# Kernel tuning notes

Hardware: AMD Instinct MI355X
Metric: run time of the kernel (lower is better)

Reference implementation:

```python
import jax, jax.numpy as jnp
import numpy as np

N_TX, N_ACC, N_MER = 100000, 50000, 5000
HID, HEADS, OUT_CH, LAYERS = 128, 4, 64, 3
HC = HID * HEADS  # 512, concat-heads width
SRC_T = ['tx', 'tx', 'tx', 'acc', 'acc', 'mer']
DST_T = ['acc', 'acc', 'mer', 'tx', 'tx', 'tx']


def setup_inputs():
    key = jax.random.key(0)
    ks = jax.random.split(key, 16)
    rn = lambda k, s: jax.random.normal(k, s, dtype=jnp.float32) * 0.05
    n_of = {'tx': N_TX, 'acc': N_ACC, 'mer': N_MER}
    E = N_TX  # one sender-acct / receiver-acct / merchant edge per transaction
    src = jnp.stack([jax.random.randint(jax.random.fold_in(ks[0], r), (E,), 0, n_of[SRC_T[r]]) for r in range(6)])
    dst = jnp.stack([jax.random.randint(jax.random.fold_in(ks[1], r), (E,), 0, n_of[DST_T[r]]) for r in range(6)])
    edges = jnp.stack([src, dst], axis=1).astype(jnp.int32)  # [6, 2, E] (rel, src/dst, edge)
    return dict(
        x_tx=rn(ks[2], (N_TX, 64)), x_acc=rn(ks[3], (N_ACC, 32)), x_mer=rn(ks[4], (N_MER, 32)),
        Wtx=rn(ks[5], (64, HID)), btx=jnp.zeros((HID,), jnp.float32),
        Wacc=rn(ks[6], (32, HID)), bacc=jnp.zeros((HID,), jnp.float32),
        Wmer=rn(ks[7], (32, HID)), bmer=jnp.zeros((HID,), jnp.float32),
        W0=rn(ks[8], (6, HID, HC)),            # layer-0 GAT linear per relation
        Wrest=rn(ks[9], (LAYERS - 1, 6, HC, HC)),  # layers 1..L-1
        att_s=rn(ks[10], (LAYERS, 6, HEADS, HID)),
        att_d=rn(ks[11], (LAYERS, 6, HEADS, HID)),
        att_b=jnp.zeros((LAYERS, 6, HC), jnp.float32),
        bn_g=jnp.ones((LAYERS, HC), jnp.float32), bn_b=jnp.zeros((LAYERS, HC), jnp.float32),
        Wh1=rn(ks[12], (HC, OUT_CH)), bh1=jnp.zeros((OUT_CH,), jnp.float32),
        Wh2=rn(ks[13], (OUT_CH, 1)), bh2=jnp.zeros((1,), jnp.float32),
        edges=edges)


def _gat_rel(x_src, x_dst, src, dst, W, a_s, a_d, b, n_dst):
    """PyG GATConv (shared lin, add_self_loops=False, concat heads), eval mode."""
    H, C = a_s.shape
    hs = (x_src @ W).reshape(-1, H, C)  # [Ns, H, C]
    hd = (x_dst @ W).reshape(-1, H, C)  # [Nd, H, C]
    e = jax.nn.leaky_relu((hs * a_s).sum(-1)[src] + (hd * a_d).sum(-1)[dst], 0.2)  # [E, H]
    m = jax.lax.stop_gradient(jax.ops.segment_max(e, dst, num_segments=n_dst))
    ex = jnp.exp(e - m[dst])
    denom = jax.ops.segment_sum(ex, dst, num_segments=n_dst)
    alpha = ex / (denom[dst] + 1e-16)  # segment softmax over in-edges of each dst
    out = jax.ops.segment_sum(alpha[:, :, None] * hs[src], dst, num_segments=n_dst)
    return out.reshape(n_dst, H * C) + b


def _forward(x_tx, x_acc, x_mer, Wtx, btx, Wacc, bacc, Wmer, bmer, W0, Wrest,
             att_s, att_d, att_b, bn_g, bn_b, Wh1, bh1, Wh2, bh2, edges):
    h = {'tx': jax.nn.relu(x_tx @ Wtx + btx),
         'acc': jax.nn.relu(x_acc @ Wacc + bacc),
         'mer': jax.nn.relu(x_mer @ Wmer + bmer)}
    n_of = {'tx': x_tx.shape[0], 'acc': x_acc.shape[0], 'mer': x_mer.shape[0]}
    for i in range(LAYERS):
        Wl = W0 if i == 0 else Wrest[i - 1]
        new = {k: jnp.zeros((n_of[k], HC), x_tx.dtype) for k in n_of}  # HeteroConv aggr='sum'
        for r in range(6):
            o = _gat_rel(h[SRC_T[r]], h[DST_T[r]], edges[r, 0], edges[r, 1],
                         Wl[r], att_s[i, r], att_d[i, r], att_b[i, r], n_of[DST_T[r]])
            new[DST_T[r]] = new[DST_T[r]] + o
        t = new['tx']  # BatchNorm1d (batch statistics) on transaction nodes only
        mu = t.mean(0)
        var = t.var(0)
        new['tx'] = (t - mu) / jnp.sqrt(var + 1e-5) * bn_g[i] + bn_b[i]
        new = {k: jax.nn.relu(v) for k, v in new.items()}
        if i > 0:  # residual from second layer on
            new = {k: new[k] + h[k] for k in new}
        h = new
    hidden = jax.nn.relu(h['tx'] @ Wh1 + bh1)
    return (hidden @ Wh2 + bh2).squeeze(-1)  # [N_tx] logits


def reference(x_tx, x_acc, x_mer, Wtx, btx, Wacc, bacc, Wmer, bmer, W0, Wrest,
              att_s, att_d, att_b, bn_g, bn_b, Wh1, bh1, Wh2, bh2, edges):
    return _forward(x_tx, x_acc, x_mer, Wtx, btx, Wacc, bacc, Wmer, bmer, W0, Wrest,
                    att_s, att_d, att_b, bn_g, bn_b, Wh1, bh1, Wh2, bh2, edges)
```

## Files before the change

### kernel.cpp

```cpp
#include <hip/hip_runtime.h>
#include <math.h>


typedef unsigned short BF16;
typedef short short8 __attribute__((ext_vector_type(8)));
typedef float f32x4 __attribute__((ext_vector_type(4)));
typedef __bf16 bf16x8 __attribute__((ext_vector_type(8)));

static __device__ __forceinline__ float lrelu(float x){ return x > 0.f ? x : 0.2f*x; }

__device__ __forceinline__ float ldE(const float* p, long i){ return p[i]; }
__device__ __forceinline__ float ldE(const BF16* p, long i){
  return __uint_as_float((unsigned)p[i] << 16);
}
__device__ __forceinline__ void stE(float* p, long i, float v){ p[i] = v; }
__device__ __forceinline__ void stE(BF16* p, long i, float v){
  unsigned u = __float_as_uint(v);
  p[i] = (BF16)((u + 0x7FFFu + ((u >> 16) & 1u)) >> 16);
}
__device__ __forceinline__ BF16 f2bf(float v){
  unsigned u = __float_as_uint(v);
  return (BF16)((u + 0x7FFFu + ((u >> 16) & 1u)) >> 16);
}
__device__ __forceinline__ float bf2f(short s){
  return __uint_as_float((unsigned)(unsigned short)s << 16);
}
__device__ __forceinline__ float4 ld4E(const float* p, long i){ return *(const float4*)(p + i); }
__device__ __forceinline__ float4 ld4E(const BF16* p, long i){
  ushort4 s = *(const ushort4*)(p + i);
  return make_float4(__uint_as_float((unsigned)s.x<<16), __uint_as_float((unsigned)s.y<<16),
                     __uint_as_float((unsigned)s.z<<16), __uint_as_float((unsigned)s.w<<16));
}

__global__ void k_zero(int* __restrict__ p, long n){
  long i = (long)blockIdx.x*blockDim.x + threadIdx.x;
  if (i < n) p[i] = 0;
}
__global__ void k_fill_f32(float* __restrict__ p, long n, float v){
  long i = (long)blockIdx.x*blockDim.x + threadIdx.x;
  if (i < n) p[i] = v;
}

__global__ __launch_bounds__(256) void k_wt(const float* __restrict__ in, BF16* __restrict__ out,
                                            int K, int N)
{
  __shared__ float t[32][33];
  int kb = blockIdx.y*32, nb = blockIdx.x*32;
  int tx = threadIdx.x & 31, ty8 = threadIdx.x >> 5;
  for (int j = ty8; j < 32; j += 8){
    int k = kb + j, n = nb + tx;
    t[j][tx] = (k < K && n < N) ? in[(long)k*N + n] : 0.f;
  }
  __syncthreads();
  for (int j = ty8; j < 32; j += 8){
    int n = nb + j, k = kb + tx;
    if (n < N && k < K) out[(long)n*K + k] = f2bf(t[tx][j]);
  }
}

template<int BN, int WM, int WN, int FM, int FN, typename TC>
__global__ __launch_bounds__(256) void k_mfma(
    const BF16* __restrict__ A, const BF16* __restrict__ Bt, TC* __restrict__ C,
    int M, int K, int c0, int ldc, const float* __restrict__ bias, int doRelu)
{
  constexpr int BM = 128;
  constexpr int LSTR = 72;
  __shared__ __attribute__((aligned(16))) short Als[BM][LSTR];
  __shared__ __attribute__((aligned(16))) short Bls[BN][LSTR];
  const int bm = blockIdx.y*BM;
  const int tid = threadIdx.x;
  const int wave = tid >> 6, lane = tid & 63;
  const int wr = wave / WN, wc = wave % WN;
  const int lrow = lane & 15, kg = lane >> 4;
  f32x4 acc[FM][FN] = {};
  for (int k0 = 0; k0 < K; k0 += 64){
    #pragma unroll
    for (int t = 0; t < 4; ++t){
      int idx = tid + t*256;
      int row = idx >> 3, kc = (idx & 7) << 3;
      int gr = bm + row;
      short8 v = {};
      if (gr < M) v = *(const short8*)(A + (long)gr*K + k0 + kc);
      *(short8*)&Als[row][kc] = v;
    }
    #pragma unroll
    for (int t = 0; t < BN/32; ++t){
      int idx = tid + t*256;
      int row = idx >> 3, kc = (idx & 7) << 3;
      *(short8*)&Bls[row][kc] = *(const short8*)(Bt + (long)(c0+row)*K + k0 + kc);
    }
    __syncthreads();
    #pragma unroll
    for (int kk = 0; kk < 2; ++kk){
      short8 af[FM], bq[FN];
      #pragma unroll
      for (int m = 0; m < FM; ++m)
        af[m] = *(const short8*)&Als[wr*FM*16 + m*16 + lrow][kk*32 + kg*8];
      #pragma unroll
      for (int n = 0; n < FN; ++n)
        bq[n] = *(const short8*)&Bls[wc*FN*16 + n*16 + lrow][kk*32 + kg*8];
      #pragma unroll
      for (int m = 0; m < FM; ++m)
        #pragma unroll
        for (int n = 0; n < FN; ++n)
          acc[m][n] = __builtin_amdgcn_mfma_f32_16x16x32_bf16(
              __builtin_bit_cast(bf16x8, af[m]), __builtin_bit_cast(bf16x8, bq[n]),
              acc[m][n], 0, 0, 0);
    }
    __syncthreads();
  }
  #pragma unroll
  for (int m = 0; m < FM; ++m){
    #pragma unroll
    for (int n = 0; n < FN; ++n){
      #pragma unroll
      for (int j = 0; j < 4; ++j){
        int row = bm + wr*FM*16 + m*16 + kg*4 + j;
        if (row >= M) continue;
        int col = wc*FN*16 + n*16 + lrow;
        float v = acc[m][n][j];
        if (bias) v += bias[col];
        if (doRelu) v = fmaxf(v, 0.f);
        stE(C, (long)row*ldc + col, v);
      }
    }
  }
}

template<typename TA, typename TC>
__global__ __launch_bounds__(256) void k_gemm(
    const TA* __restrict__ A, const float* __restrict__ B, TC* __restrict__ C,
    int M, int N, int K, int ldb, const float* __restrict__ bias, int doRelu)
{
  __shared__ float As[16][64];
  __shared__ float Bs[16][64];
  const int bm = blockIdx.y*64, bn = blockIdx.x*64;
  const int tid = threadIdx.x;
  const int ty = tid >> 4, tx = tid & 15;
  const int ar = tid >> 2;
  const int ac = (tid & 3) << 2;
  const int br = tid >> 4;
  const int bc = (tid & 15) << 2;
  float acc[4][4] = {};
  for (int k0 = 0; k0 < K; k0 += 16){
    int row = bm + ar;
    float4 av = make_float4(0.f,0.f,0.f,0.f);
    if (row < M) av = ld4E(A, (long)row*K + k0 + ac);
    As[ac+0][ar]=av.x; As[ac+1][ar]=av.y; As[ac+2][ar]=av.z; As[ac+3][ar]=av.w;
    float4 bv = make_float4(0.f,0.f,0.f,0.f);
    if (bn + bc + 3 < N) bv = *(const float4*)(B + (long)(k0+br)*ldb + bn + bc);
    *(float4*)&Bs[br][bc] = bv;
    __syncthreads();
    #pragma unroll
    for (int kk = 0; kk < 16; ++kk){
      float a[4], b[4];
      #pragma unroll
      for (int x = 0; x < 4; ++x){ a[x]=As[kk][ty*4+x]; b[x]=Bs[kk][tx*4+x]; }
      #pragma unroll
      for (int y = 0; y < 4; ++y)
        #pragma unroll
        for (int x = 0; x < 4; ++x) acc[y][x] += a[y]*b[x];
    }
    __syncthreads();
  }
  #pragma unroll
  for (int y = 0; y < 4; ++y){
    int row = bm + ty*4 + y;
    if (row >= M) continue;
    #pragma unroll
    for (int x = 0; x < 4; ++x){
      int col = bn + tx*4 + x;
      if (col >= N) continue;
      float v = acc[y][x];
      if (bias) v += bias[col];
      if (doRelu) v = fmaxf(v, 0.f);
      stE(C, (long)row*N + col, v);
    }
  }
}

__global__ void k_fold(const float* __restrict__ W, const float* __restrict__ att,
                       float* __restrict__ F, int Din)
{
  int idx = blockIdx.x*blockDim.x + threadIdx.x;
  if (idx >= 4*Din) return;
  int h = idx / Din, k = idx % Din;
  float s = 0.f;
  const float* wr = W + (long)k*512 + h*128;
  const float* ar = att + h*128;
  for (int c = 0; c < 128; ++c) s += wr[c]*ar[c];
  F[h*Din + k] = s;
}

__global__ __launch_bounds__(256) void k_score4(
    const BF16* __restrict__ X, const float* __restrict__ F,
    float* __restrict__ out, int N, int Din)
{
  __shared__ float Fs[2048];
  for (int i = threadIdx.x; i < 4*Din; i += 256) Fs[i] = F[i];
  __syncthreads();
  int wave = threadIdx.x >> 6, lane = threadIdx.x & 63;
  int base = lane*8;
  bool act = base < Din;
  float f0[8], f1[8], f2[8], f3[8];
  if (act){
    #pragma unroll
    for (int j = 0; j < 8; ++j){
      f0[j] = Fs[0*Din + base + j];
      f1[j] = Fs[1*Din + base + j];
      f2[j] = Fs[2*Din + base + j];
      f3[j] = Fs[3*Din + base + j];
    }
  }
  #pragma unroll
  for (int t = 0; t < 4; ++t){
    int node = blockIdx.x*16 + wave*4 + t;
    if (node >= N) break;
    float p0=0.f, p1=0.f, p2=0.f, p3=0.f;
    if (act){
      short8 v = *(const short8*)(X + (long)node*Din + base);
      #pragma unroll
      for (int j = 0; j < 8; ++j){
        float x = bf2f(v[j]);
        p0 += x*f0[j]; p1 += x*f1[j]; p2 += x*f2[j]; p3 += x*f3[j];
      }
    }
    #pragma unroll
    for (int off = 32; off; off >>= 1){
      p0 += __shfl_down(p0, off, 64);
      p1 += __shfl_down(p1, off, 64);
      p2 += __shfl_down(p2, off, 64);
      p3 += __shfl_down(p3, off, 64);
    }
    if (lane == 0){
      out[(long)node*4 + 0] = p0;
      out[(long)node*4 + 1] = p1;
      out[(long)node*4 + 2] = p2;
      out[(long)node*4 + 3] = p3;
    }
  }
}

__global__ void k_hist(const int* __restrict__ dst, int* __restrict__ counts, int E, int nd){
  int e = blockIdx.x*blockDim.x + threadIdx.x;
  if (e >= E) return;
  int d = dst[e];
  if ((unsigned)d < (unsigned)nd) atomicAdd(&counts[d], 1);
}
__global__ void k_scan1(const int* __restrict__ counts, int* __restrict__ indptr,
                        int* __restrict__ bsums, int n)
{
  __shared__ int sm[256];
  int i = blockIdx.x*256 + threadIdx.x;
  int v = (i < n) ? counts[i] : 0;
  sm[threadIdx.x] = v; __syncthreads();
  for (int off = 1; off < 256; off <<= 1){
    int t = (threadIdx.x >= off) ? sm[threadIdx.x - off] : 0;
    __syncthreads();
    sm[threadIdx.x] += t;
    __syncthreads();
  }
  if (i < n) indptr[i+1] = sm[threadIdx.x];
  if (threadIdx.x == 255) bsums[blockIdx.x] = sm[255];
  if (blockIdx.x == 0 && threadIdx.x == 0) indptr[0] = 0;
}
__global__ void k_scan2(int* __restrict__ bsums, int nb){
  __shared__ int sm[1024];
  int t = threadIdx.x;
  int v = (t < nb) ? bsums[t] : 0;
  sm[t] = v; __syncthreads();
  for (int off = 1; off < 1024; off <<= 1){
    int x = (t >= off) ? sm[t - off] : 0;
    __syncthreads();
    sm[t] += x;
    __syncthreads();
  }
  if (t < nb) bsums[t] = sm[t];
}
__global__ void k_scan3(int* __restrict__ indptr, const int* __restrict__ bsums, int n){
  if (blockIdx.x == 0) return;
  int i = blockIdx.x*256 + threadIdx.x;
  int add = bsums[blockIdx.x - 1];
  if (i < n) indptr[i+1] += add;
}
__global__ void k_scatter(const int* __restrict__ src, const int* __restrict__ dst,
                          const int* __restrict__ indptr, int* __restrict__ cursor,
                          int* __restrict__ esrc, int E, int nd, int ns)
{
  int e = blockIdx.x*blockDim.x + threadIdx.x;
  if (e >= E) return;
  int d = dst[e];
  if ((unsigned)d >= (unsigned)nd) return;
  int s = src[e];
  if ((unsigned)s >= (unsigned)ns) s = 0;
  int pos = indptr[d] + atomicAdd(&cursor[d], 1);
  if (pos >= 0 && pos < E) esrc[pos] = s;
}

__global__ __launch_bounds__(256) void k_alpha(
    const float* __restrict__ ss, const float* __restrict__ sd,
    const int* __restrict__ indptr, const int* __restrict__ esrc,
    float* __restrict__ alpha, int n_dst, int E, int ns)
{
  int wid = (blockIdx.x*blockDim.x + threadIdx.x) >> 6;
  int lane = threadIdx.x & 63;
  if (wid >= n_dst) return;
  int e0 = indptr[wid], e1 = indptr[wid+1];
  e0 = max(0, min(e0, E)); e1 = max(e0, min(e1, E));
  if (e0 >= e1) return;
  int h = lane >> 4, g = lane & 15;
  float sdl = sd[(long)wid*4 + h];
  float m = -INFINITY;
  for (int e = e0 + g; e < e1; e += 16){
    int s = esrc[e]; if ((unsigned)s >= (unsigned)ns) s = 0;
    m = fmaxf(m, lrelu(ss[(long)s*4 + h] + sdl));
  }
  #pragma unroll
  for (int o = 1; o < 16; o <<= 1) m = fmaxf(m, __shfl_xor(m, o, 16));
  float den = 0.f;
  for (int e = e0 + g; e < e1; e += 16){
    int s = esrc[e]; if ((unsigned)s >= (unsigned)ns) s = 0;
    den += __expf(lrelu(ss[(long)s*4 + h] + sdl) - m);
  }
  #pragma unroll
  for (int o = 1; o < 16; o <<= 1) den += __shfl_xor(den, o, 16);
  float inv = 1.f/(den + 1e-16f);
  for (int e = e0 + g; e < e1; e += 16){
    int s = esrc[e]; if ((unsigned)s >= (unsigned)ns) s = 0;
    alpha[(long)e*4 + h] = __expf(lrelu(ss[(long)s*4 + h] + sdl) - m) * inv;
  }
}

template<int NJ>
__global__ __launch_bounds__(256) void k_agg(
    const BF16* __restrict__ Zt, const float* __restrict__ alpha,
    const int* __restrict__ indptr, const int* __restrict__ esrc,
    BF16* __restrict__ out, int ldc, int c0w, int TW, int head0,
    int accum, int n_dst, int E, int ns)
{
  int wid = (blockIdx.x*blockDim.x + threadIdx.x) >> 6;
  int lane = threadIdx.x & 63;
  if (wid >= n_dst) return;
  int e0 = indptr[wid], e1 = indptr[wid+1];
  e0 = max(0, min(e0, E)); e1 = max(e0, min(e1, E));
  float acc[NJ];
  #pragma unroll
  for (int j = 0; j < NJ; ++j) acc[j] = 0.f;
  for (int e = e0; e < e1; ++e){
    int s = esrc[e]; if ((unsigned)s >= (unsigned)ns) s = 0;
    float aA = alpha[(long)e*4 + head0];
    float aB = (NJ == 4) ? alpha[(long)e*4 + head0 + 1] : aA;
    const BF16* zr = Zt + (long)s*TW;
    #pragma unroll
    for (int j = 0; j < NJ; ++j){
      int col = lane + 64*j;
      if (col < TW){
        float a = (NJ == 4 && j >= 2) ? aB : aA;
        acc[j] += a * ldE(zr, col);
      }
    }
  }
  #pragma unroll
  for (int j = 0; j < NJ; ++j){
    int col = lane + 64*j;
    if (col < TW){
      long idx = (long)wid*ldc + c0w + col;
      float v = acc[j];
      if (accum) v += ldE(out, idx);
      stE(out, idx, v);
    }
  }
}

__global__ void k_bnp(const BF16* __restrict__ nw, float* __restrict__ bnp,
                      int N, int TW, int P)
{
  int col  = threadIdx.x & (TW - 1);
  int slot = threadIdx.x / TW;
  int rpb  = 256 / TW;
  int p    = blockIdx.x*rpb + slot;
  float s = 0.f, s2 = 0.f;
  for (long r = p; r < N; r += P){
    float v = ldE(nw, r*TW + col);
    s += v; s2 += v*v;
  }
  bnp[(long)p*2*TW + col]      = s;
  bnp[(long)p*2*TW + TW + col] = s2;
}
__global__ void k_bnf(const float* __restrict__ bnp, float* __restrict__ bns,
                      int P, int TW)
{
  for (int c = threadIdx.x; c < 2*TW; c += 256){
    float s = 0.f;
    for (int p = 0; p < P; ++p) s += bnp[(long)p*2*TW + c];
    bns[c] = s;
  }
}
__global__ void k_bn_apply(const BF16* __restrict__ nw, const float* __restrict__ bns,
                           const float* __restrict__ g, const float* __restrict__ b,
                           BF16* __restrict__ A, int N, int TW, int c0, int res)
{
  long total = (long)N*TW;
  for (long i = (long)blockIdx.x*blockDim.x + threadIdx.x; i < total;
       i += (long)gridDim.x*blockDim.x){
    int col = (int)(i % TW);
    long r  = i / TW;
    float mu  = bns[col] / (float)N;
    float var = bns[TW + col] / (float)N - mu*mu;
    int gc = c0 + col;
    float sc = g[gc] * rsqrtf(var + 1e-5f);
    float sh = b[gc] - mu*sc;
    float v = fmaxf(ldE(nw, i)*sc + sh, 0.f);
    long ai = r*512 + gc;
    if (res) v += ldE(A, ai);
    stE(A, ai, v);
  }
}

__global__ void k_update(const BF16* __restrict__ B, const float* __restrict__ ab1,
                         const float* __restrict__ ab2, BF16* __restrict__ A,
                         long n512, int res)
{
  for (long i = (long)blockIdx.x*blockDim.x + threadIdx.x; i < n512;
       i += (long)gridDim.x*blockDim.x){
    int c = (int)(i & 511);
    float v = ldE(B, i) + ab1[c] + (ab2 ? ab2[c] : 0.f);
    v = fmaxf(v, 0.f);
    if (res) v += ldE(A, i);
    stE(A, i, v);
  }
}

__global__ void k_logits(const BF16* __restrict__ Hid, const float* __restrict__ Wh2,
                         const float* __restrict__ bh2, float* __restrict__ out, int N)
{
  int node = (blockIdx.x*blockDim.x + threadIdx.x) >> 6;
  int lane = threadIdx.x & 63;
  if (node >= N) return;
  float v = ldE(Hid, (long)node*64 + lane) * Wh2[lane];
  #pragma unroll
  for (int off = 32; off; off >>= 1) v += __shfl_down(v, off, 64);
  if (lane == 0) out[node] = v + bh2[0];
}

struct Arena {
  BF16 *A[3];
  BF16 *Bst[3];
  BF16 *Zt;
  BF16 *nwtile;
  BF16 *hidden;
  float *alpha;
  float *ss, *sd, *fs, *fd, *bnp, *bns;
  int *counts, *bsums;
  int *indptr[6], *esrc[6];
  BF16 *Wt0[6], *WtL[2][6], *Wh1t;
  size_t total;
};

extern "C" void kernel_launch(void* const* d_in, const int* in_sizes, int n_in,
                              void* d_out, int out_size, void* d_ws, size_t ws_size,
                              hipStream_t stream)
{
  const float* x_tx  = (const float*)d_in[0];
  const float* x_acc = (const float*)d_in[1];
  const float* x_mer = (const float*)d_in[2];
  const float* Wtx = (const float*)d_in[3];  const float* btx  = (const float*)d_in[4];
  const float* Wacc= (const float*)d_in[5];  const float* bacc = (const float*)d_in[6];
  const float* Wmer= (const float*)d_in[7];  const float* bmer = (const float*)d_in[8];
  const float* W0   = (const float*)d_in[9];
  const float* Wrest= (const float*)d_in[10];
  const float* att_s= (const float*)d_in[11];
  const float* att_d= (const float*)d_in[12];
  const float* att_b= (const float*)d_in[13];
  const float* bn_g = (const float*)d_in[14];
  const float* bn_b = (const float*)d_in[15];
  const float* Wh1  = (const float*)d_in[16]; const float* bh1 = (const float*)d_in[17];
  const float* Wh2  = (const float*)d_in[18]; const float* bh2 = (const float*)d_in[19];
  const int*   edges= (const int*)d_in[20];

  const int E    = in_sizes[20] / 12;
  const int nTx  = in_sizes[0] / 64;
  const int nAcc = in_sizes[1] / 32;
  const int nMer = in_sizes[2] / 32;
  const int nOf[3]   = {nTx, nAcc, nMer};
  const int SRC_T[6] = {0,0,0,1,1,2};
  const int DST_T[6] = {1,1,2,0,0,0};
  const int maxN = max(nTx, max(nAcc, nMer));
  (void)n_in;

  auto layout = [&](int TW)->Arena{
    Arena P{};
    size_t off = 0;
    auto a = [&](size_t bytes)->char*{
      char* p = (char*)d_ws + off;
      off += (bytes + 255) & ~(size_t)255;
      return p;
    };
    auto al = [](size_t b){ return (b + 255) & ~(size_t)255; };
    P.A[0]   = (BF16*)a((size_t)nTx *512*2);
    P.A[1]   = (BF16*)a((size_t)nAcc*512*2);
    P.A[2]   = (BF16*)a((size_t)nMer*512*2);
    P.Bst[1] = (BF16*)a((size_t)nAcc*512*2);
    P.Bst[2] = (BF16*)a((size_t)nMer*512*2);
    size_t zB  = al((size_t)maxN*TW*2);
    size_t nwB = al((size_t)nTx*TW*2);
    size_t hidB= al((size_t)nTx*64*2);
    size_t scr = zB + nwB;
    char* scrBase = a(scr > hidB ? scr : hidB);
    P.Zt     = (BF16*)scrBase;
    P.nwtile = (BF16*)(scrBase + zB);
    P.hidden = (BF16*)scrBase;
    P.alpha  = (float*)a((size_t)3*E*4*4);
    P.ss     = (float*)a((size_t)maxN*4*4);
    P.sd     = (float*)a((size_t)maxN*4*4);
    P.fs     = (float*)a(4*512*4);
    P.fd     = (float*)a(4*512*4);
    P.bnp    = (float*)a(262144);
    P.bns    = (float*)a(4096);
    P.counts = (int*)a((size_t)maxN*4);
    P.bsums  = (int*)a(4096);
    for (int r = 0; r < 6; ++r){
      P.indptr[r] = (int*)a((size_t)(nOf[DST_T[r]]+1)*4);
      P.esrc[r]   = (int*)a((size_t)E*4);
    }
    for (int r = 0; r < 6; ++r) P.Wt0[r] = (BF16*)a((size_t)512*128*2);
    for (int l = 0; l < 2; ++l)
      for (int r = 0; r < 6; ++r) P.WtL[l][r] = (BF16*)a((size_t)512*512*2);
    P.Wh1t = (BF16*)a((size_t)64*512*2);
    P.total = off;
    return P;
  };

  int TW = 0;
  Arena P{};
  for (int cand : {256, 128, 64, 32}){
    P = layout(cand);
    if (P.total <= ws_size){ TW = cand; break; }
  }
  if (TW == 0){
    float sentinel = 10000.0f + (float)(ws_size >> 20);
    k_fill_f32<<<dim3((out_size+255)/256), dim3(256), 0, stream>>>((float*)d_out, (long)out_size, sentinel);
    return;
  }
  const int nTiles = 512 / TW;
  const int rpb = 256 / TW, PBX = 128, Pp = PBX * rpb;
  dim3 b256(256);

  for (int r = 0; r < 6; ++r)
    k_wt<<<dim3(16,4), b256, 0, stream>>>(W0 + (size_t)r*128*512, P.Wt0[r], 128, 512);
  for (int l = 0; l < 2; ++l)
    for (int r = 0; r < 6; ++r)
      k_wt<<<dim3(16,16), b256, 0, stream>>>(Wrest + ((size_t)l*6 + r)*512*512, P.WtL[l][r], 512, 512);
  k_wt<<<dim3(2,16), b256, 0, stream>>>(Wh1, P.Wh1t, 512, 64);

  auto mfma_gemm = [&](const BF16* A, const BF16* Bt, BF16* Cp, int M, int K, int c0){
    dim3 g(1, (M+127)/128);
    if (TW >= 128){
      for (int ch = 0; ch < TW; ch += 128)
        k_mfma<128,2,2,4,4,BF16><<<g,b256,0,stream>>>(A, Bt, Cp + ch, M, K, c0 + ch, TW, (const float*)nullptr, 0);
    } else if (TW == 64){
      k_mfma<64,4,1,2,4,BF16><<<g,b256,0,stream>>>(A, Bt, Cp, M, K, c0, TW, (const float*)nullptr, 0);
    } else {
      k_mfma<32,4,1,2,2,BF16><<<g,b256,0,stream>>>(A, Bt, Cp, M, K, c0, TW, (const float*)nullptr, 0);
    }
  };
  auto agg = [&](const BF16* Zt, const float* al, const int* ip, const int* es,
                 BF16* out, int ldc, int c0w, int head0, int accum, int nd, int ns){
    dim3 g((nd+3)/4);
    if (TW == 256)      k_agg<4><<<g,b256,0,stream>>>(Zt, al, ip, es, out, ldc, c0w, TW, head0, accum, nd, E, ns);
    else if (TW == 128) k_agg<2><<<g,b256,0,stream>>>(Zt, al, ip, es, out, ldc, c0w, TW, head0, accum, nd, E, ns);
    else                k_agg<1><<<g,b256,0,stream>>>(Zt, al, ip, es, out, ldc, c0w, TW, head0, accum, nd, E, ns);
  };

  for (int r = 0; r < 6; ++r){
    int nd = nOf[DST_T[r]], ns = nOf[SRC_T[r]];
    const int* srcP = edges + (size_t)r*2*E;
    const int* dstP = srcP + E;
    int nb = (nd + 255)/256;
    k_zero   <<<dim3(nb),          b256, 0, stream>>>(P.counts, (long)nd);
    k_hist   <<<dim3((E+255)/256), b256, 0, stream>>>(dstP, P.counts, E, nd);
    k_scan1  <<<dim3(nb),          b256, 0, stream>>>(P.counts, P.indptr[r], P.bsums, nd);
    k_scan2  <<<dim3(1),           dim3(1024),0, stream>>>(P.bsums, nb);
    k_scan3  <<<dim3(nb),          b256, 0, stream>>>(P.indptr[r], P.bsums, nd);
    k_zero   <<<dim3(nb),          b256, 0, stream>>>(P.counts, (long)nd);
    k_scatter<<<dim3((E+255)/256), b256, 0, stream>>>(srcP, dstP, P.indptr[r], P.counts, P.esrc[r], E, nd, ns);
  }

  k_gemm<float,BF16><<<dim3(2,(nTx +63)/64), b256, 0, stream>>>(x_tx,  Wtx,  P.A[0], nTx,  128, 64, 128, btx,  1);
  k_gemm<float,BF16><<<dim3(2,(nAcc+63)/64), b256, 0, stream>>>(x_acc, Wacc, P.A[1], nAcc, 128, 32, 128, bacc, 1);
  k_gemm<float,BF16><<<dim3(2,(nMer+63)/64), b256, 0, stream>>>(x_mer, Wmer, P.A[2], nMer, 128, 32, 128, bmer, 1);

  for (int i = 0; i < 3; ++i){
    const int Din = (i == 0) ? 128 : 512;
    const int res = (i > 0) ? 1 : 0;
    auto Wof = [&](int r)->const float*{
      return (i == 0) ? (W0 + (size_t)r*128*512)
                      : (Wrest + ((size_t)(i-1)*6 + r)*512*512);
    };
    auto Wtof = [&](int r)->const BF16*{
      return (i == 0) ? P.Wt0[r] : P.WtL[i-1][r];
    };
    for (int r = 0; r < 3; ++r){
      int dt = DST_T[r];
      int nd = nOf[dt];
      const float* as_ = att_s + ((size_t)(i*6 + r))*4*128;
      const float* ad_ = att_d + ((size_t)(i*6 + r))*4*128;
      k_fold<<<dim3((4*Din+255)/256), b256, 0, stream>>>(Wof(r), as_, P.fs, Din);
      k_fold<<<dim3((4*Din+255)/256), b256, 0, stream>>>(Wof(r), ad_, P.fd, Din);
      k_score4<<<dim3((nTx+15)/16), b256, 0, stream>>>(P.A[0], P.fs, P.ss, nTx, Din);
      k_score4<<<dim3((nd+15)/16),  b256, 0, stream>>>(P.A[dt], P.fd, P.sd, nd, Din);
      k_alpha<<<dim3((nd+3)/4), b256, 0, stream>>>(P.ss, P.sd, P.indptr[r], P.esrc[r],
                                                   P.alpha, nd, E, nTx);
      int accF = (r == 1) ? 1 : 0;
      for (int t = 0; t < nTiles; ++t){
        int c0 = t*TW;
        mfma_gemm(P.A[0], Wtof(r), P.Zt, nTx, Din, c0);
        agg(P.Zt, P.alpha, P.indptr[r], P.esrc[r], P.Bst[dt], 512, c0, c0 >> 7, accF, nd, nTx);
      }
    }
    for (int r = 3; r < 6; ++r){
      int st = SRC_T[r];
      int ns = nOf[st];
      const float* as_ = att_s + ((size_t)(i*6 + r))*4*128;
      const float* ad_ = att_d + ((size_t)(i*6 + r))*4*128;
      k_fold<<<dim3((4*Din+255)/256), b256, 0, stream>>>(Wof(r), as_, P.fs, Din);
      k_fold<<<dim3((4*Din+255)/256), b256, 0, stream>>>(Wof(r), ad_, P.fd, Din);
      k_score4<<<dim3((ns+15)/16),  b256, 0, stream>>>(P.A[st], P.fs, P.ss, ns, Din);
      k_score4<<<dim3((nTx+15)/16), b256, 0, stream>>>(P.A[0],  P.fd, P.sd, nTx, Din);
      k_alpha<<<dim3((nTx+3)/4), b256, 0, stream>>>(P.ss, P.sd, P.indptr[r], P.esrc[r],
                                                    P.alpha + (size_t)(r-3)*E*4, nTx, E, ns);
    }
    for (int t = 0; t < nTiles; ++t){
      int c0 = t*TW;
      for (int r = 3; r < 6; ++r){
        int st = SRC_T[r], ns = nOf[st];
        mfma_gemm(P.A[st], Wtof(r), P.Zt, ns, Din, c0);
        agg(P.Zt, P.alpha + (size_t)(r-3)*E*4, P.indptr[r], P.esrc[r],
            P.nwtile, TW, 0, c0 >> 7, (r > 3) ? 1 : 0, nTx, ns);
      }
      k_bnp<<<dim3(PBX), b256, 0, stream>>>(P.nwtile, P.bnp, nTx, TW, Pp);
      k_bnf<<<dim3(1),   b256, 0, stream>>>(P.bnp, P.bns, Pp, TW);
      k_bn_apply<<<dim3(2048), b256, 0, stream>>>(P.nwtile, P.bns,
          bn_g + (size_t)i*512, bn_b + (size_t)i*512, P.A[0], nTx, TW, c0, res);
    }
    const float* ab0 = att_b + ((size_t)(i*6 + 0))*512;
    const float* ab1 = att_b + ((size_t)(i*6 + 1))*512;
    const float* ab2 = att_b + ((size_t)(i*6 + 2))*512;
    k_update<<<dim3(2048), b256, 0, stream>>>(P.Bst[1], ab0, ab1, P.A[1], (long)nAcc*512, res);
    k_update<<<dim3(256),  b256, 0, stream>>>(P.Bst[2], ab2, (const float*)nullptr, P.A[2], (long)nMer*512, res);
  }

  k_mfma<64,4,1,2,4,BF16><<<dim3(1,(nTx+127)/128), b256, 0, stream>>>(
      P.A[0], P.Wh1t, P.hidden, nTx, 512, 0, 64, bh1, 1);
  k_logits<<<dim3((nTx+3)/4), b256, 0, stream>>>(P.hidden, Wh2, bh2, (float*)d_out, nTx);
}
```

Before: 12.16 ms.

## Batch attention folds and scores, fuse three tx-destination aggregations into one kernel

```diff
diff --git a/kernel.cpp b/kernel.cpp
--- a/kernel.cpp
+++ b/kernel.cpp
@@ -58,6 +58,26 @@
   }
 }
 
+__global__ __launch_bounds__(256) void k_foldAll(
+    const float* __restrict__ Wbase, long wstride,
+    const float* __restrict__ atts, const float* __restrict__ attd,
+    float* __restrict__ F, int Din)
+{
+  int w = (blockIdx.x*256 + threadIdx.x) >> 6;
+  int lane = threadIdx.x & 63;
+  int total = 48*Din;
+  if (w >= total) return;
+  int k = w % Din;
+  int rem = w / Din;
+  int h = rem & 3, sd = (rem >> 2) & 1, r = rem >> 3;
+  const float* wr = Wbase + (long)r*wstride + (long)k*512 + h*128;
+  const float* ar = (sd ? attd : atts) + r*512 + h*128;
+  float p = wr[lane]*ar[lane] + wr[lane+64]*ar[lane+64];
+  #pragma unroll
+  for (int off = 32; off; off >>= 1) p += __shfl_down(p, off, 64);
+  if (lane == 0) F[(long)((r*2+sd)*4 + h)*Din + k] = p;
+}
+
 template<int BN, int WM, int WN, int FM, int FN, typename TC>
 __global__ __launch_bounds__(256) void k_mfma(
     const BF16* __restrict__ A, const BF16* __restrict__ Bt, TC* __restrict__ C,
@@ -67,6 +87,7 @@
   constexpr int LSTR = 72;
   __shared__ __attribute__((aligned(16))) short Als[BM][LSTR];
   __shared__ __attribute__((aligned(16))) short Bls[BN][LSTR];
+  const int bn0 = blockIdx.x * BN;
   const int bm = blockIdx.y*BM;
   const int tid = threadIdx.x;
   const int wave = tid >> 6, lane = tid & 63;
@@ -87,7 +108,7 @@
     for (int t = 0; t < BN/32; ++t){
       int idx = tid + t*256;
       int row = idx >> 3, kc = (idx & 7) << 3;
-      *(short8*)&Bls[row][kc] = *(const short8*)(Bt + (long)(c0+row)*K + k0 + kc);
+      *(short8*)&Bls[row][kc] = *(const short8*)(Bt + (long)(c0+bn0+row)*K + k0 + kc);
     }
     __syncthreads();
     #pragma unroll
@@ -119,9 +140,9 @@
         if (row >= M) continue;
         int col = wc*FN*16 + n*16 + lrow;
         float v = acc[m][n][j];
-        if (bias) v += bias[col];
+        if (bias) v += bias[bn0 + col];
         if (doRelu) v = fmaxf(v, 0.f);
-        stE(C, (long)row*ldc + col, v);
+        stE(C, (long)row*ldc + bn0 + col, v);
       }
     }
   }
@@ -179,64 +200,67 @@
   }
 }
 
-__global__ void k_fold(const float* __restrict__ W, const float* __restrict__ att,
-                       float* __restrict__ F, int Din)
-{
-  int idx = blockIdx.x*blockDim.x + threadIdx.x;
-  if (idx >= 4*Din) return;
-  int h = idx / Din, k = idx % Din;
-  float s = 0.f;
-  const float* wr = W + (long)k*512 + h*128;
-  const float* ar = att + h*128;
-  for (int c = 0; c < 128; ++c) s += wr[c]*ar[c];
-  F[h*Din + k] = s;
-}
-
-__global__ __launch_bounds__(256) void k_score4(
-    const BF16* __restrict__ X, const float* __restrict__ F,
-    float* __restrict__ out, int N, int Din)
-{
-  __shared__ float Fs[2048];
-  for (int i = threadIdx.x; i < 4*Din; i += 256) Fs[i] = F[i];
-  __syncthreads();
+template<int R>
+__global__ __launch_bounds__(256) void k_scoreM(
+    const BF16* __restrict__ X, const float* __restrict__ Ftab, long fstride,
+    float* __restrict__ out, long ostride, int N, int Din)
+{
   int wave = threadIdx.x >> 6, lane = threadIdx.x & 63;
+  int node0 = blockIdx.x*16 + wave*4;
+  if (node0 >= N) return;
   int base = lane*8;
   bool act = base < Din;
-  float f0[8], f1[8], f2[8], f3[8];
-  if (act){
+  float x[4][8];
+  #pragma unroll
+  for (int t = 0; t < 4; ++t){
+    int node = node0 + t;
+    if (act && node < N){
+      short8 v = *(const short8*)(X + (long)node*Din + base);
+      #pragma unroll
+      for (int j = 0; j < 8; ++j) x[t][j] = bf2f(v[j]);
+    } else {
+      #pragma unroll
+      for (int j = 0; j < 8; ++j) x[t][j] = 0.f;
+    }
+  }
+  #pragma unroll
+  for (int r = 0; r < R; ++r){
+    const float* F = Ftab + (long)r*fstride;
+    float p[4][4] = {};
     #pragma unroll
-    for (int j = 0; j < 8; ++j){
-      f0[j] = Fs[0*Din + base + j];
-      f1[j] = Fs[1*Din + base + j];
-      f2[j] = Fs[2*Din + base + j];
-      f3[j] = Fs[3*Din + base + j];
-    }
-  }
-  #pragma unroll
-  for (int t = 0; t < 4; ++t){
-    int node = blockIdx.x*16 + wave*4 + t;
-    if (node >= N) break;
-    float p0=0.f, p1=0.f, p2=0.f, p3=0.f;
-    if (act){
-      short8 v = *(const short8*)(X + (long)node*Din + base);
-      #pragma unroll
-      for (int j = 0; j < 8; ++j){
-        float x = bf2f(v[j]);
-        p0 += x*f0[j]; p1 += x*f1[j]; p2 += x*f2[j]; p3 += x*f3[j];
+    for (int h = 0; h < 4; ++h){
+      float f[8];
+      if (act){
+        float4 fa = *(const float4*)(F + h*Din + base);
+        float4 fb = *(const float4*)(F + h*Din + base + 4);
+        f[0]=fa.x; f[1]=fa.y; f[2]=fa.z; f[3]=fa.w;
+        f[4]=fb.x; f[5]=fb.y; f[6]=fb.z; f[7]=fb.w;
+      } else {
+        #pragma unroll
+        for (int j = 0; j < 8; ++j) f[j] = 0.f;
       }
+      #pragma unroll
+      for (int t = 0; t < 4; ++t)
+        #pragma unroll
+        for (int j = 0; j < 8; ++j) p[t][h] += x[t][j]*f[j];
     }
     #pragma unroll
-    for (int off = 32; off; off >>= 1){
-      p0 += __shfl_down(p0, off, 64);
-      p1 += __shfl_down(p1, off, 64);
-      p2 += __shfl_down(p2, off, 64);
-      p3 += __shfl_down(p3, off, 64);
-    }
+    for (int t = 0; t < 4; ++t)
+      #pragma unroll
+      for (int h = 0; h < 4; ++h)
+        #pragma unroll
+        for (int off = 32; off; off >>= 1)
+          p[t][h] += __shfl_down(p[t][h], off, 64);
     if (lane == 0){
-      out[(long)node*4 + 0] = p0;
-      out[(long)node*4 + 1] = p1;
-      out[(long)node*4 + 2] = p2;
-      out[(long)node*4 + 3] = p3;
+      #pragma unroll
+      for (int t = 0; t < 4; ++t){
+        int node = node0 + t;
+        if (node < N){
+          #pragma unroll
+          for (int h = 0; h < 4; ++h)
+            out[(long)r*ostride + (long)node*4 + h] = p[t][h];
+        }
+      }
     }
   }
 }
@@ -331,6 +355,25 @@
   }
 }
 
+__device__ __forceinline__ void agg_body(
+    const BF16* __restrict__ Zt, const float* __restrict__ alpha,
+    const int* __restrict__ indptr, const int* __restrict__ esrc,
+    float* acc, int NJ, int wid, int lane, int TW, int head0, int E, int ns)
+{
+  int e0 = indptr[wid], e1 = indptr[wid+1];
+  e0 = max(0, min(e0, E)); e1 = max(e0, min(e1, E));
+  for (int e = e0; e < e1; ++e){
+    int s = esrc[e]; if ((unsigned)s >= (unsigned)ns) s = 0;
+    float aA = alpha[(long)e*4 + head0];
+    float aB = (NJ == 4) ? alpha[(long)e*4 + head0 + 1] : aA;
+    const BF16* zr = Zt + (long)s*TW;
+    #pragma unroll 4
+    for (int j = 0; j < NJ; ++j){
+      int col = lane + 64*j;
+      if (col < TW) acc[j] += ((NJ == 4 && j >= 2) ? aB : aA) * ldE(zr, col);
+    }
+  }
+}
 template<int NJ>
 __global__ __launch_bounds__(256) void k_agg(
     const BF16* __restrict__ Zt, const float* __restrict__ alpha,
@@ -341,25 +384,10 @@
   int wid = (blockIdx.x*blockDim.x + threadIdx.x) >> 6;
   int lane = threadIdx.x & 63;
   if (wid >= n_dst) return;
-  int e0 = indptr[wid], e1 = indptr[wid+1];
-  e0 = max(0, min(e0, E)); e1 = max(e0, min(e1, E));
   float acc[NJ];
   #pragma unroll
   for (int j = 0; j < NJ; ++j) acc[j] = 0.f;
-  for (int e = e0; e < e1; ++e){
-    int s = esrc[e]; if ((unsigned)s >= (unsigned)ns) s = 0;
-    float aA = alpha[(long)e*4 + head0];
-    float aB = (NJ == 4) ? alpha[(long)e*4 + head0 + 1] : aA;
-    const BF16* zr = Zt + (long)s*TW;
-    #pragma unroll
-    for (int j = 0; j < NJ; ++j){
-      int col = lane + 64*j;
-      if (col < TW){
-        float a = (NJ == 4 && j >= 2) ? aB : aA;
-        acc[j] += a * ldE(zr, col);
-      }
-    }
-  }
+  agg_body(Zt, alpha, indptr, esrc, acc, NJ, wid, lane, TW, head0, E, ns);
   #pragma unroll
   for (int j = 0; j < NJ; ++j){
     int col = lane + 64*j;
@@ -369,6 +397,31 @@
       if (accum) v += ldE(out, idx);
       stE(out, idx, v);
     }
+  }
+}
+
+template<int NJ>
+__global__ __launch_bounds__(256) void k_agg3(
+    const BF16* __restrict__ Z0, const BF16* __restrict__ Z1, const BF16* __restrict__ Z2,
+    const float* __restrict__ a0, const float* __restrict__ a1, const float* __restrict__ a2,
+    const int* __restrict__ ip0, const int* __restrict__ ip1, const int* __restrict__ ip2,
+    const int* __restrict__ es0, const int* __restrict__ es1, const int* __restrict__ es2,
+    BF16* __restrict__ out, int ldc, int TW, int head0,
+    int n_dst, int E, int ns0, int ns1, int ns2)
+{
+  int wid = (blockIdx.x*blockDim.x + threadIdx.x) >> 6;
+  int lane = threadIdx.x & 63;
+  if (wid >= n_dst) return;
+  float acc[NJ];
+  #pragma unroll
+  for (int j = 0; j < NJ; ++j) acc[j] = 0.f;
+  agg_body(Z0, a0, ip0, es0, acc, NJ, wid, lane, TW, head0, E, ns0);
+  agg_body(Z1, a1, ip1, es1, acc, NJ, wid, lane, TW, head0, E, ns1);
+  agg_body(Z2, a2, ip2, es2, acc, NJ, wid, lane, TW, head0, E, ns2);
+  #pragma unroll
+  for (int j = 0; j < NJ; ++j){
+    int col = lane + 64*j;
+    if (col < TW) stE(out, (long)wid*ldc + col, acc[j]);
   }
 }
 
@@ -390,11 +443,11 @@
 __global__ void k_bnf(const float* __restrict__ bnp, float* __restrict__ bns,
                       int P, int TW)
 {
-  for (int c = threadIdx.x; c < 2*TW; c += 256){
-    float s = 0.f;
-    for (int p = 0; p < P; ++p) s += bnp[(long)p*2*TW + c];
-    bns[c] = s;
-  }
+  int c = blockIdx.x*256 + threadIdx.x;
+  if (c >= 2*TW) return;
+  float s = 0.f;
+  for (int p = 0; p < P; ++p) s += bnp[(long)p*2*TW + c];
+  bns[c] = s;
 }
 __global__ void k_bn_apply(const BF16* __restrict__ nw, const float* __restrict__ bns,
                            const float* __restrict__ g, const float* __restrict__ b,
@@ -449,8 +502,10 @@
   BF16 *Zt;
   BF16 *nwtile;
   BF16 *hidden;
+  float *scoreS, *scoreD;
   float *alpha;
-  float *ss, *sd, *fs, *fd, *bnp, *bns;
+  float *Fbuf;
+  float *bnp, *bns;
   int *counts, *bsums;
   int *indptr[6], *esrc[6];
   BF16 *Wt0[6], *WtL[2][6], *Wh1t;
@@ -502,19 +557,22 @@
     P.A[2]   = (BF16*)a((size_t)nMer*512*2);
     P.Bst[1] = (BF16*)a((size_t)nAcc*512*2);
     P.Bst[2] = (BF16*)a((size_t)nMer*512*2);
-    size_t zB  = al((size_t)maxN*TW*2);
+    size_t zrows = (size_t)maxN > (size_t)2*nAcc + nMer ? (size_t)maxN : (size_t)2*nAcc + nMer;
+    size_t zB  = al(zrows*TW*2);
     size_t nwB = al((size_t)nTx*TW*2);
+    size_t scoreB = al((size_t)3*maxN*4*4)*2;
     size_t hidB= al((size_t)nTx*64*2);
     size_t scr = zB + nwB;
-    char* scrBase = a(scr > hidB ? scr : hidB);
+    if (scr < scoreB) scr = scoreB;
+    if (scr < hidB)   scr = hidB;
+    char* scrBase = a(scr);
     P.Zt     = (BF16*)scrBase;
     P.nwtile = (BF16*)(scrBase + zB);
+    P.scoreS = (float*)scrBase;
+    P.scoreD = (float*)(scrBase + al((size_t)3*maxN*4*4));
     P.hidden = (BF16*)scrBase;
     P.alpha  = (float*)a((size_t)3*E*4*4);
-    P.ss     = (float*)a((size_t)maxN*4*4);
-    P.sd     = (float*)a((size_t)maxN*4*4);
-    P.fs     = (float*)a(4*512*4);
-    P.fd     = (float*)a(4*512*4);
+    P.Fbuf   = (float*)a((size_t)6*8*512*4);
     P.bnp    = (float*)a(262144);
     P.bns    = (float*)a(4096);
     P.counts = (int*)a((size_t)maxN*4);
@@ -533,7 +591,7 @@
 
   int TW = 0;
   Arena P{};
-  for (int cand : {256, 128, 64, 32}){
+  for (int cand : {256, 128, 64}){
     P = layout(cand);
     if (P.total <= ws_size){ TW = cand; break; }
   }
@@ -543,6 +601,7 @@
     return;
   }
   const int nTiles = 512 / TW;
+  const int NJv = TW/64;
   const int rpb = 256 / TW, PBX = 128, Pp = PBX * rpb;
   dim3 b256(256);
 
@@ -553,23 +612,18 @@
       k_wt<<<dim3(16,16), b256, 0, stream>>>(Wrest + ((size_t)l*6 + r)*512*512, P.WtL[l][r], 512, 512);
   k_wt<<<dim3(2,16), b256, 0, stream>>>(Wh1, P.Wh1t, 512, 64);
 
-  auto mfma_gemm = [&](const BF16* A, const BF16* Bt, BF16* Cp, int M, int K, int c0){
-    dim3 g(1, (M+127)/128);
-    if (TW >= 128){
-      for (int ch = 0; ch < TW; ch += 128)
-        k_mfma<128,2,2,4,4,BF16><<<g,b256,0,stream>>>(A, Bt, Cp + ch, M, K, c0 + ch, TW, (const float*)nullptr, 0);
-    } else if (TW == 64){
-      k_mfma<64,4,1,2,4,BF16><<<g,b256,0,stream>>>(A, Bt, Cp, M, K, c0, TW, (const float*)nullptr, 0);
-    } else {
-      k_mfma<32,4,1,2,2,BF16><<<g,b256,0,stream>>>(A, Bt, Cp, M, K, c0, TW, (const float*)nullptr, 0);
-    }
+  auto mfma_gemm = [&](const BF16* A, const BF16* Bt, BF16* Cp, int M, int K, int c0, int ldc){
+    if (TW >= 128)
+      k_mfma<128,2,2,4,4,BF16><<<dim3(TW/128,(M+127)/128),b256,0,stream>>>(A, Bt, Cp, M, K, c0, ldc, (const float*)nullptr, 0);
+    else
+      k_mfma<64,4,1,2,4,BF16><<<dim3(1,(M+127)/128),b256,0,stream>>>(A, Bt, Cp, M, K, c0, ldc, (const float*)nullptr, 0);
   };
-  auto agg = [&](const BF16* Zt, const float* al, const int* ip, const int* es,
-                 BF16* out, int ldc, int c0w, int head0, int accum, int nd, int ns){
+  auto agg1 = [&](const BF16* Zt, const float* al, const int* ip, const int* es,
+                  BF16* out, int ldc, int c0w, int head0, int accum, int nd, int ns){
     dim3 g((nd+3)/4);
-    if (TW == 256)      k_agg<4><<<g,b256,0,stream>>>(Zt, al, ip, es, out, ldc, c0w, TW, head0, accum, nd, E, ns);
-    else if (TW == 128) k_agg<2><<<g,b256,0,stream>>>(Zt, al, ip, es, out, ldc, c0w, TW, head0, accum, nd, E, ns);
-    else                k_agg<1><<<g,b256,0,stream>>>(Zt, al, ip, es, out, ldc, c0w, TW, head0, accum, nd, E, ns);
+    if (NJv == 4)      k_agg<4><<<g,b256,0,stream>>>(Zt, al, ip, es, out, ldc, c0w, TW, head0, accum, nd, E, ns);
+    else if (NJv == 2) k_agg<2><<<g,b256,0,stream>>>(Zt, al, ip, es, out, ldc, c0w, TW, head0, accum, nd, E, ns);
+    else               k_agg<1><<<g,b256,0,stream>>>(Zt, al, ip, es, out, ldc, c0w, TW, head0, accum, nd, E, ns);
   };
 
   for (int r = 0; r < 6; ++r){
@@ -590,56 +644,68 @@
   k_gemm<float,BF16><<<dim3(2,(nAcc+63)/64), b256, 0, stream>>>(x_acc, Wacc, P.A[1], nAcc, 128, 32, 128, bacc, 1);
   k_gemm<float,BF16><<<dim3(2,(nMer+63)/64), b256, 0, stream>>>(x_mer, Wmer, P.A[2], nMer, 128, 32, 128, bmer, 1);
 
+  const long mS = (long)maxN*4;
   for (int i = 0; i < 3; ++i){
     const int Din = (i == 0) ? 128 : 512;
     const int res = (i > 0) ? 1 : 0;
-    auto Wof = [&](int r)->const float*{
-      return (i == 0) ? (W0 + (size_t)r*128*512)
-                      : (Wrest + ((size_t)(i-1)*6 + r)*512*512);
-    };
-    auto Wtof = [&](int r)->const BF16*{
-      return (i == 0) ? P.Wt0[r] : P.WtL[i-1][r];
-    };
+    const long fstr = 8L*Din;
+    const float* WbaseL = (i == 0) ? W0 : (Wrest + (size_t)(i-1)*6*512*512);
+    const long wstride = (i == 0) ? 128L*512 : 512L*512;
+    auto Wtof = [&](int r)->const BF16*{ return (i == 0) ? P.Wt0[r] : P.WtL[i-1][r]; };
+
+    k_foldAll<<<dim3(48*Din/4), b256, 0, stream>>>(WbaseL, wstride,
+        att_s + (size_t)i*6*512, att_d + (size_t)i*6*512, P.Fbuf, Din);
+
+    k_scoreM<3><<<dim3((nTx+15)/16), b256, 0, stream>>>(P.A[0], P.Fbuf,           fstr, P.scoreS, mS, nTx, Din);
+    k_scoreM<2><<<dim3((nAcc+15)/16), b256, 0, stream>>>(P.A[1], P.Fbuf + 4*Din,  fstr, P.scoreD, mS, nAcc, Din);
+    k_scoreM<1><<<dim3((nMer+15)/16), b256, 0, stream>>>(P.A[2], P.Fbuf + 20*Din, fstr, P.scoreD + 2*mS, 0, nMer, Din);
     for (int r = 0; r < 3; ++r){
-      int dt = DST_T[r];
-      int nd = nOf[dt];
-      const float* as_ = att_s + ((size_t)(i*6 + r))*4*128;
-      const float* ad_ = att_d + ((size_t)(i*6 + r))*4*128;
-      k_fold<<<dim3((4*Din+255)/256), b256, 0, stream>>>(Wof(r), as_, P.fs, Din);
-      k_fold<<<dim3((4*Din+255)/256), b256, 0, stream>>>(Wof(r), ad_, P.fd, Din);
-      k_score4<<<dim3((nTx+15)/16), b256, 0, stream>>>(P.A[0], P.fs, P.ss, nTx, Din);
-      k_score4<<<dim3((nd+15)/16),  b256, 0, stream>>>(P.A[dt], P.fd, P.sd, nd, Din);
-      k_alpha<<<dim3((nd+3)/4), b256, 0, stream>>>(P.ss, P.sd, P.indptr[r], P.esrc[r],
-                                                   P.alpha, nd, E, nTx);
+      int nd = nOf[DST_T[r]];
+      k_alpha<<<dim3((nd+3)/4), b256, 0, stream>>>(P.scoreS + r*mS, P.scoreD + r*mS,
+          P.indptr[r], P.esrc[r], P.alpha + (size_t)r*E*4, nd, E, nTx);
+    }
+    for (int r = 0; r < 3; ++r){
+      int dt = DST_T[r], nd = nOf[dt];
       int accF = (r == 1) ? 1 : 0;
       for (int t = 0; t < nTiles; ++t){
         int c0 = t*TW;
-        mfma_gemm(P.A[0], Wtof(r), P.Zt, nTx, Din, c0);
-        agg(P.Zt, P.alpha, P.indptr[r], P.esrc[r], P.Bst[dt], 512, c0, c0 >> 7, accF, nd, nTx);
+        mfma_gemm(P.A[0], Wtof(r), P.Zt, nTx, Din, c0, TW);
+        agg1(P.Zt, P.alpha + (size_t)r*E*4, P.indptr[r], P.esrc[r],
+             P.Bst[dt], 512, c0, c0 >> 7, accF, nd, nTx);
       }
     }
-    for (int r = 3; r < 6; ++r){
-      int st = SRC_T[r];
-      int ns = nOf[st];
-      const float* as_ = att_s + ((size_t)(i*6 + r))*4*128;
-      const float* ad_ = att_d + ((size_t)(i*6 + r))*4*128;
-      k_fold<<<dim3((4*Din+255)/256), b256, 0, stream>>>(Wof(r), as_, P.fs, Din);
-      k_fold<<<dim3((4*Din+255)/256), b256, 0, stream>>>(Wof(r), ad_, P.fd, Din);
-      k_score4<<<dim3((ns+15)/16),  b256, 0, stream>>>(P.A[st], P.fs, P.ss, ns, Din);
-      k_score4<<<dim3((nTx+15)/16), b256, 0, stream>>>(P.A[0],  P.fd, P.sd, nTx, Din);
-      k_alpha<<<dim3((nTx+3)/4), b256, 0, stream>>>(P.ss, P.sd, P.indptr[r], P.esrc[r],
-                                                    P.alpha + (size_t)(r-3)*E*4, nTx, E, ns);
-    }
+
+    k_scoreM<2><<<dim3((nAcc+15)/16), b256, 0, stream>>>(P.A[1], P.Fbuf + 24*Din, fstr, P.scoreS, mS, nAcc, Din);
+    k_scoreM<1><<<dim3((nMer+15)/16), b256, 0, stream>>>(P.A[2], P.Fbuf + 40*Din, fstr, P.scoreS + 2*mS, 0, nMer, Din);
+    k_scoreM<3><<<dim3((nTx+15)/16), b256, 0, stream>>>(P.A[0], P.Fbuf + 28*Din, fstr, P.scoreD, mS, nTx, Din);
+    for (int q = 0; q < 3; ++q){
+      int r = 3 + q;
+      k_alpha<<<dim3((nTx+3)/4), b256, 0, stream>>>(P.scoreS + q*mS, P.scoreD + q*mS,
+          P.indptr[r], P.esrc[r], P.alpha + (size_t)q*E*4, nTx, E, nOf[SRC_T[r]]);
+    }
+    BF16* Z3 = P.Zt;
+    BF16* Z4 = P.Zt + (size_t)nAcc*TW;
+    BF16* Z5 = P.Zt + (size_t)2*nAcc*TW;
     for (int t = 0; t < nTiles; ++t){
       int c0 = t*TW;
-      for (int r = 3; r < 6; ++r){
-        int st = SRC_T[r], ns = nOf[st];
-        mfma_gemm(P.A[st], Wtof(r), P.Zt, ns, Din, c0);
-        agg(P.Zt, P.alpha + (size_t)(r-3)*E*4, P.indptr[r], P.esrc[r],
-            P.nwtile, TW, 0, c0 >> 7, (r > 3) ? 1 : 0, nTx, ns);
-      }
+      mfma_gemm(P.A[1], Wtof(3), Z3, nAcc, Din, c0, TW);
+      mfma_gemm(P.A[1], Wtof(4), Z4, nAcc, Din, c0, TW);
+      mfma_gemm(P.A[2], Wtof(5), Z5, nMer, Din, c0, TW);
+      dim3 ga((nTx+3)/4);
+      if (NJv == 4)
+        k_agg3<4><<<ga,b256,0,stream>>>(Z3,Z4,Z5, P.alpha, P.alpha+(size_t)E*4, P.alpha+(size_t)2*E*4,
+            P.indptr[3],P.indptr[4],P.indptr[5], P.esrc[3],P.esrc[4],P.esrc[5],
+            P.nwtile, TW, TW, c0>>7, nTx, E, nAcc, nAcc, nMer);
+      else if (NJv == 2)
+        k_agg3<2><<<ga,b256,0,stream>>>(Z3,Z4,Z5, P.alpha, P.alpha+(size_t)E*4, P.alpha+(size_t)2*E*4,
+            P.indptr[3],P.indptr[4],P.indptr[5], P.esrc[3],P.esrc[4],P.esrc[5],
+            P.nwtile, TW, TW, c0>>7, nTx, E, nAcc, nAcc, nMer);
+      else
+        k_agg3<1><<<ga,b256,0,stream>>>(Z3,Z4,Z5, P.alpha, P.alpha+(size_t)E*4, P.alpha+(size_t)2*E*4,
+            P.indptr[3],P.indptr[4],P.indptr[5], P.esrc[3],P.esrc[4],P.esrc[5],
+            P.nwtile, TW, TW, c0>>7, nTx, E, nAcc, nAcc, nMer);
       k_bnp<<<dim3(PBX), b256, 0, stream>>>(P.nwtile, P.bnp, nTx, TW, Pp);
-      k_bnf<<<dim3(1),   b256, 0, stream>>>(P.bnp, P.bns, Pp, TW);
+      k_bnf<<<dim3((2*TW+255)/256), b256, 0, stream>>>(P.bnp, P.bns, Pp, TW);
       k_bn_apply<<<dim3(2048), b256, 0, stream>>>(P.nwtile, P.bns,
           bn_g + (size_t)i*512, bn_b + (size_t)i*512, P.A[0], nTx, TW, c0, res);
     }
```

Result: faster. 11.54 ms (-5.1%).
